# Kernel optimization log

Hardware: AMD Instinct MI355X
Metric: run time of the kernel (lower is better)

Reference implementation:

```python
import jax, jax.numpy as jnp
import numpy as np

LN_EPS = 1e-5


def _ln(x, g, b):
    m = jnp.mean(x, axis=-1, keepdims=True)
    v = jnp.mean((x - m) ** 2, axis=-1, keepdims=True)
    return (x - m) / jnp.sqrt(v + LN_EPS) * g + b


def setup_inputs() -> dict:
    key = jax.random.key(0)
    ks = jax.random.split(key, 8)
    B, N, S, D, T = 16, 64, 2048, 1024, 768

    def xavier(k, shape):
        fan_in, fan_out = shape
        lim = (6.0 / (fan_in + fan_out)) ** 0.5
        return jax.random.uniform(k, shape, minval=-lim, maxval=lim, dtype=jnp.float32)

    return {
        "prev_states": jax.random.normal(ks[0], (B, N, D), dtype=jnp.float32),
        "input_tokens": jax.random.normal(ks[1], (B, S, T), dtype=jnp.float32),
        # input_projection (token_dim -> state_dim)
        "W_proj": xavier(ks[2], (T, D)),
        "b_proj": jnp.zeros((D,), jnp.float32),
        # three LayerNorms
        "g_state": jnp.ones((D,), jnp.float32), "beta_state": jnp.zeros((D,), jnp.float32),
        "g_input": jnp.ones((D,), jnp.float32), "beta_input": jnp.zeros((D,), jnp.float32),
        "g_out": jnp.ones((D,), jnp.float32), "beta_out": jnp.zeros((D,), jnp.float32),
        # GRU gates (2D -> D); update-gate bias initialized to -1 as in the module
        "W_u": xavier(ks[3], (2 * D, D)), "b_u": jnp.full((D,), -1.0, jnp.float32),
        "W_r": xavier(ks[4], (2 * D, D)), "b_r": jnp.zeros((D,), jnp.float32),
        "W_n": xavier(ks[5], (2 * D, D)), "b_n": jnp.zeros((D,), jnp.float32),
    }


def reference(prev_states, input_tokens, W_proj, b_proj,
              g_state, beta_state, g_input, beta_input, g_out, beta_out,
              W_u, b_u, W_r, b_r, W_n, b_n):
    D = prev_states.shape[-1]
    # project tokens to state dim: (B,S,D)
    tok = input_tokens @ W_proj + b_proj
    # attention routing (routing_weights=None path)
    scores = jnp.einsum('bnd,bsd->bns', prev_states, tok) / jnp.sqrt(jnp.float32(D))
    attn = jax.nn.softmax(scores, axis=-1)
    routed = jnp.einsum('bns,bsd->bnd', attn, tok)  # (B,N,D)
    # GRU-style gated update, vectorized over the num_states axis
    ps_n = _ln(prev_states, g_state, beta_state)
    in_n = _ln(routed, g_input, beta_input)
    concat = jnp.concatenate([ps_n, in_n], axis=-1)  # (B,N,2D)
    u = jax.nn.sigmoid(concat @ W_u + b_u)
    r = jax.nn.sigmoid(concat @ W_r + b_r)
    reset_in = jnp.concatenate([r * ps_n, in_n], axis=-1)
    cand = jnp.tanh(reset_in @ W_n + b_n)  # dropout is identity in eval
    new_state = (1.0 - u) * prev_states + u * cand
    return _ln(new_state, g_out, beta_out)
```

## Files before the change

kernel.cpp:

```cpp
#include <hip/hip_runtime.h>
#include <stdint.h>

typedef __attribute__((ext_vector_type(4))) float floatx4;
typedef __attribute__((ext_vector_type(8))) short shortx8;

#define LN_EPS 1e-5f

__device__ __forceinline__ unsigned short f2b(float f) {
  unsigned u = __builtin_bit_cast(unsigned, f);
  u = (u + 0x7FFFu + ((u >> 16) & 1u)) >> 16;
  return (unsigned short)u;
}
__device__ __forceinline__ float b2f(unsigned short h) {
  return __builtin_bit_cast(float, (unsigned)h << 16);
}

__device__ __forceinline__ void g2l16(const unsigned short* g, unsigned short* l) {
  __builtin_amdgcn_global_load_lds(
      (const __attribute__((address_space(1))) unsigned int*)g,
      (__attribute__((address_space(3))) unsigned int*)l, 16, 0, 0);
}

__device__ __forceinline__ float wave_sum(float v) {
#pragma unroll
  for (int o = 32; o; o >>= 1) v += __shfl_down(v, o, 64);
  return v;
}
__device__ __forceinline__ float block_sum(float v, float* s) {
  v = wave_sum(v);
  __syncthreads();
  if ((threadIdx.x & 63) == 0) s[threadIdx.x >> 6] = v;
  __syncthreads();
  return s[0] + s[1] + s[2] + s[3];
}

__global__ __launch_bounds__(256) void k_prep_pw(
    const float* __restrict__ prev, const float* __restrict__ wp,
    const float* __restrict__ Wu, const float* __restrict__ Wr,
    const float* __restrict__ Wn,
    unsigned short* __restrict__ Wtur, unsigned short* __restrict__ Wtn,
    unsigned short* __restrict__ Wtp, unsigned short* __restrict__ pwb,
    float* __restrict__ rs) {
  __shared__ unsigned short As[2][64 * 64];
  __shared__ unsigned short Bs[2][64 * 64];
  const int bid = blockIdx.x;
  const int tid = threadIdx.x;
  if (bid < 192) {
    const int wave = tid >> 6, lane = tid & 63;
    const int swz = (bid & 7) * 24 + (bid >> 3);
    const int m0 = (swz % 16) * 64;
    const int n0 = (swz / 16) * 64;
    const int wm = wave & 1, wn = wave >> 1;
    const int l16 = lane & 15, quad = lane >> 4;
    const int srow8 = lane >> 3;
    const int c8 = ((lane & 7) ^ srow8) * 8;

    const float* gAf[2];
    const float* gBf[2];
    int lOff[2];
#pragma unroll
    for (int j = 0; j < 2; j++) {
      const int rb = wave * 16 + j * 8;
      gAf[j] = prev + (long)(m0 + rb + srow8) * 1024 + c8;
      gBf[j] = wp + (long)(n0 + rb + srow8) * 1024 + c8;
      lOff[j] = rb * 64;
    }
    int offA[2][2], offB[2][2];
#pragma unroll
    for (int ks = 0; ks < 2; ks++)
#pragma unroll
      for (int i = 0; i < 2; i++) {
        int r = wm * 32 + i * 16 + l16;
        offA[ks][i] = r * 64 + (((ks * 4 + quad) ^ (r & 7)) * 8);
        r = wn * 32 + i * 16 + l16;
        offB[ks][i] = r * 64 + (((ks * 4 + quad) ^ (r & 7)) * 8);
// ... 41 lines not shown
        for (int j = 0; j < 2; j++) bf[j] = *(const shortx8*)&Bs[cur][offB[ks][j]];
#pragma unroll
        for (int i = 0; i < 2; i++)
#pragma unroll
          for (int j = 0; j < 2; j++)
            acc[i][j] = __builtin_amdgcn_mfma_f32_16x16x32_bf16(af[i], bf[j], acc[i][j], 0, 0, 0);
      }
      if (t + 1 < nt) {
#pragma unroll
        for (int j = 0; j < 2; j++) {
          unsigned short ta[8], tb[8];
#pragma unroll
          for (int i = 0; i < 4; i++) {
            ta[i] = f2b(a0[j][i]); ta[4 + i] = f2b(a1[j][i]);
            tb[i] = f2b(b0[j][i]); tb[4 + i] = f2b(b1[j][i]);
          }
          *(uint4*)&As[cur ^ 1][lOff[j] + lane * 8] = *(uint4*)ta;
          *(uint4*)&Bs[cur ^ 1][lOff[j] + lane * 8] = *(uint4*)tb;
        }
      }
      __syncthreads();
    }

#pragma unroll
    for (int i = 0; i < 2; i++)
#pragma unroll
      for (int j = 0; j < 2; j++) {
        const int rbase = m0 + wm * 32 + i * 16 + quad * 4;
        const int c = n0 + wn * 32 + j * 16 + l16;
#pragma unroll
        for (int r = 0; r < 4; r++)
          pwb[(long)(rbase + r) * 768 + c] = f2b(acc[i][j][r]);
      }
    return;
  }
  float(*tile)[33] = (float(*)[33]) & As[0][0];
  if (bid == 192) {
    floatx4 z = {0.f, 0.f, 0.f, 0.f};
    *(floatx4*)(rs + tid * 4) = z;
  }
  int t = bid - 192;
  const float* in;
  unsigned short* out;
  int K, kx, ny;
  if (t < 6144) {
    const int which = t >> 11;
    const int t2 = t & 2047;
    kx = t2 & 63;
    ny = t2 >> 6;
    K = 2048;
    in = which == 0 ? Wu : (which == 1 ? Wr : Wn);
    out = which == 0 ? Wtur : (which == 1 ? Wtur + 1024 * 2048 : Wtn);
  } else {
    const int t2 = t - 6144;
    kx = t2 % 24;
    ny = t2 / 24;
    K = 768;
    in = wp;
    out = Wtp;
  }
  const int N = 1024;
  const int k0 = kx * 32, n0 = ny * 32;
  const int tx = tid & 31, ty = tid >> 5;
#pragma unroll
  for (int i = 0; i < 32; i += 8)
    tile[ty + i][tx] = in[(long)(k0 + ty + i) * N + n0 + tx];
  __syncthreads();
#pragma unroll
  for (int i = 0; i < 32; i += 8)
    out[(long)(n0 + ty + i) * K + k0 + tx] = f2b(tile[tx][ty + i]);
}

__global__ __launch_bounds__(256) void k_gemm64(
    const unsigned short* __restrict__ A, int lda,
    const unsigned short* __restrict__ Bt, int ldb,
    int K, long sCk,
    float* __restrict__ out, int ldc) {
  __shared__ unsigned short As[2][64 * 64];
  __shared__ unsigned short Bs[2][64 * 64];
  const int tid = threadIdx.x;
  const int wave = tid >> 6, lane = tid & 63;
  const int kc = blockIdx.z;
  const long koff = (long)kc * K;
  const int flat = blockIdx.x + blockIdx.y * gridDim.x;
  const int q = (gridDim.x * gridDim.y) >> 3;
  const int swz = (flat & 7) * q + (flat >> 3);
  const int m0 = (swz % gridDim.x) * 64;
  const int n0 = (swz / gridDim.x) * 64;
  const int wm = wave & 1, wn = wave >> 1;
  const int l16 = lane & 15, quad = lane >> 4;
  const int srow8 = lane >> 3;
  const int c8 = ((lane & 7) ^ srow8) * 8;

  const unsigned short* gA[2];
  const unsigned short* gB[2];
  int lOff[2];
#pragma unroll
  for (int j = 0; j < 2; j++) {
    const int rb = wave * 16 + j * 8;
    gA[j] = A + (long)(m0 + rb + srow8) * lda + c8 + koff;
    gB[j] = Bt + (long)(n0 + rb + srow8) * ldb + c8 + koff;
    lOff[j] = rb * 64;
  }
  int offA[2][2], offB[2][2];
#pragma unroll
  for (int ks = 0; ks < 2; ks++)
#pragma unroll
    for (int i = 0; i < 2; i++) {
      int r = wm * 32 + i * 16 + l16;
      offA[ks][i] = r * 64 + (((ks * 4 + quad) ^ (r & 7)) * 8);
      r = wn * 32 + i * 16 + l16;
      offB[ks][i] = r * 64 + (((ks * 4 + quad) ^ (r & 7)) * 8);
    }

  floatx4 acc[2][2] = {};

#pragma unroll
  for (int j = 0; j < 2; j++) {
    g2l16(gA[j], &As[0][lOff[j]]);
    g2l16(gB[j], &Bs[0][lOff[j]]);
  }
  __syncthreads();

  const int nt = K >> 6;
  for (int t = 0; t < nt; t++) {
    const int cur = t & 1;
    if (t + 1 < nt) {
      const int kn = (t + 1) << 6;
#pragma unroll
      for (int j = 0; j < 2; j++) {
        g2l16(gA[j] + kn, &As[cur ^ 1][lOff[j]]);
        g2l16(gB[j] + kn, &Bs[cur ^ 1][lOff[j]]);
      }
    }
#pragma unroll
    for (int ks = 0; ks < 2; ks++) {
      shortx8 af[2], bf[2];
#pragma unroll
      for (int i = 0; i < 2; i++) af[i] = *(const shortx8*)&As[cur][offA[ks][i]];
#pragma unroll
      for (int j = 0; j < 2; j++) bf[j] = *(const shortx8*)&Bs[cur][offB[ks][j]];
#pragma unroll
      for (int i = 0; i < 2; i++)
#pragma unroll
        for (int j = 0; j < 2; j++)
          acc[i][j] = __builtin_amdgcn_mfma_f32_16x16x32_bf16(af[i], bf[j], acc[i][j], 0, 0, 0);
    }
    __syncthreads();
  }

#pragma unroll
  for (int i = 0; i < 2; i++)
#pragma unroll
    for (int j = 0; j < 2; j++) {
      const int rbase = m0 + wm * 32 + i * 16 + quad * 4;
      const int c = n0 + wn * 32 + j * 16 + l16;
#pragma unroll
      for (int r = 0; r < 4; r++)
        out[(long)kc * sCk + (long)(rbase + r) * ldc + c] = acc[i][j][r];
    }
}

__global__ __launch_bounds__(256) void k_proj2_ln(
    const float* __restrict__ P0, int lda,
    const unsigned short* __restrict__ Bt, int ldb,
    int K,
    const float* __restrict__ bp, const float* __restrict__ rowsum,
    float* __restrict__ out, int ldc,
    const float* __restrict__ prev,
    const float* __restrict__ g_st, const float* __restrict__ be_st,
    unsigned short* __restrict__ conc) {
  __shared__ unsigned short As[2][64 * 64];
  __shared__ unsigned short Bs[2][64 * 64];
  const int tid = threadIdx.x;
  if (blockIdx.x >= 256) {
    float* scr = (float*)&As[0][0];
    const long r = blockIdx.x - 256;
    floatx4 v = *(const floatx4*)(prev + r * 1024 + tid * 4);
    float s1 = v[0] + v[1] + v[2] + v[3];
    float s2 = v[0] * v[0] + v[1] * v[1] + v[2] * v[2] + v[3] * v[3];
    s1 = block_sum(s1, scr);
    s2 = block_sum(s2, scr);
    const float mean = s1 * (1.0f / 1024.0f);
    const float var = s2 * (1.0f / 1024.0f) - mean * mean;
    const float rstd = rsqrtf(var + LN_EPS);
    unsigned short t4[4];
#pragma unroll
    for (int i = 0; i < 4; i++) {
      const int d = tid * 4 + i;
      t4[i] = f2b((v[i] - mean) * rstd * g_st[d] + be_st[d]);
    }
    *(uint2*)(conc + r * 2048 + tid * 4) = *(uint2*)t4;
    return;
  }
  const int wave = tid >> 6, lane = tid & 63;
  const int flat = blockIdx.x;
  const int swz = (flat & 7) * 32 + (flat >> 3);
  const int m0 = (swz % 16) * 64;
  const int n0 = (swz / 16) * 64;
  const int wm = wave & 1, wn = wave >> 1;
  const int l16 = lane & 15, quad = lane >> 4;
  const int srow8 = lane >> 3;
  const int c8 = ((lane & 7) ^ srow8) * 8;

  const float* gAf[2];
  const unsigned short* gB[2];
  int lOff[2];
#pragma unroll
  for (int j = 0; j < 2; j++) {
    const int rb = wave * 16 + j * 8;
    gAf[j] = P0 + (long)(m0 + rb + srow8) * lda + c8;
    gB[j] = Bt + (long)(n0 + rb + srow8) * ldb + c8;
    lOff[j] = rb * 64;
  }
  int offA[2][2], offB[2][2];
#pragma unroll
  for (int ks = 0; ks < 2; ks++)
#pragma unroll
    for (int i = 0; i < 2; i++) {
      int r = wm * 32 + i * 16 + l16;
      offA[ks][i] = r * 64 + (((ks * 4 + quad) ^ (r & 7)) * 8);
      r = wn * 32 + i * 16 + l16;
      offB[ks][i] = r * 64 + (((ks * 4 + quad) ^ (r & 7)) * 8);
    }

  floatx4 acc[2][2] = {};

#pragma unroll
  for (int j = 0; j < 2; j++) {
    g2l16(gB[j], &Bs[0][lOff[j]]);
    floatx4 a0 = *(const floatx4*)(gAf[j]);
    floatx4 a1 = *(const floatx4*)(gAf[j] + 4);
    floatx4 b0 = *(const floatx4*)(gAf[j] + 786432);
    floatx4 b1 = *(const floatx4*)(gAf[j] + 786432 + 4);
    unsigned short t8[8];
#pragma unroll
    for (int i = 0; i < 4; i++) { t8[i] = f2b(a0[i] + b0[i]); t8[4 + i] = f2b(a1[i] + b1[i]); }
    *(uint4*)&As[0][lOff[j] + lane * 8] = *(uint4*)t8;
  }
  __syncthreads();

  const int nt = K >> 6;
  for (int t = 0; t < nt; t++) {
    const int cur = t & 1;
    floatx4 a0[2], a1[2], p0[2], p1[2];
    if (t + 1 < nt) {
      const int kn = (t + 1) << 6;
#pragma unroll
      for (int j = 0; j < 2; j++) {
        g2l16(gB[j] + kn, &Bs[cur ^ 1][lOff[j]]);
        a0[j] = *(const floatx4*)(gAf[j] + kn);
        a1[j] = *(const floatx4*)(gAf[j] + kn + 4);
        p0[j] = *(const floatx4*)(gAf[j] + kn + 786432);
        p1[j] = *(const floatx4*)(gAf[j] + kn + 786432 + 4);
      }
    }
#pragma unroll
    for (int ks = 0; ks < 2; ks++) {
      shortx8 af[2], bf[2];
#pragma unroll
      for (int i = 0; i < 2; i++) af[i] = *(const shortx8*)&As[cur][offA[ks][i]];
#pragma unroll
      for (int j = 0; j < 2; j++) bf[j] = *(const shortx8*)&Bs[cur][offB[ks][j]];
#pragma unroll
      for (int i = 0; i < 2; i++)
#pragma unroll
        for (int j = 0; j < 2; j++)
          acc[i][j] = __builtin_amdgcn_mfma_f32_16x16x32_bf16(af[i], bf[j], acc[i][j], 0, 0, 0);
    }
    if (t + 1 < nt) {
#pragma unroll
      for (int j = 0; j < 2; j++) {
        unsigned short t8[8];
#pragma unroll
        for (int i = 0; i < 4; i++) {
          t8[i] = f2b(a0[j][i] + p0[j][i]);
          t8[4 + i] = f2b(a1[j][i] + p1[j][i]);
        }
        *(uint4*)&As[cur ^ 1][lOff[j] + lane * 8] = *(uint4*)t8;
      }
    }
    __syncthreads();
  }

#pragma unroll
  for (int i = 0; i < 2; i++)
#pragma unroll
    for (int j = 0; j < 2; j++) {
      const int rbase = m0 + wm * 32 + i * 16 + quad * 4;
      const int c = n0 + wn * 32 + j * 16 + l16;
#pragma unroll
      for (int r = 0; r < 4; r++) {
        const int row = rbase + r;
        out[(long)row * ldc + c] = acc[i][j][r] + rowsum[row] * bp[c];
      }
    }
}

__global__ __launch_bounds__(256) void k_scores(
    const unsigned short* __restrict__ A, long sAb, int lda,
    const float* __restrict__ toksf,
    int K, float scale,
    unsigned short* __restrict__ out2, int ldc, long sCb,
    float* __restrict__ rs) {
  __shared__ unsigned short As[2][64 * 64];
  __shared__ unsigned short Bs[2][64 * 64];
  const int tid = threadIdx.x;
  const int wave = tid >> 6, lane = tid & 63;
  const int b = blockIdx.z;
  const int m0 = 0, n0 = blockIdx.y * 64;
  const int wm = wave & 1, wn = wave >> 1;
  const int l16 = lane & 15, quad = lane >> 4;
  const int srow8 = lane >> 3;
  const int c8 = ((lane & 7) ^ srow8) * 8;
  const unsigned short* Ab = A + (long)b * sAb;

  const unsigned short* gA[2];
  const float* gBf[2];
  int lOff[2];
#pragma unroll
  for (int j = 0; j < 2; j++) {
    const int rb = wave * 16 + j * 8;
    gA[j] = Ab + (long)(m0 + rb + srow8) * lda + c8;
    gBf[j] = toksf + (long)b * 1572864 + (long)(n0 + rb + srow8) * 768 + c8;
    lOff[j] = rb * 64;
  }
  int offA[2][2], offB[2][2];
#pragma unroll
  for (int ks = 0; ks < 2; ks++)
#pragma unroll
    for (int i = 0; i < 2; i++) {
      int r = wm * 32 + i * 16 + l16;
      offA[ks][i] = r * 64 + (((ks * 4 + quad) ^ (r & 7)) * 8);
      r = wn * 32 + i * 16 + l16;
      offB[ks][i] = r * 64 + (((ks * 4 + quad) ^ (r & 7)) * 8);
    }

  floatx4 acc[2][2] = {};

#pragma unroll
  for (int j = 0; j < 2; j++) {
    g2l16(gA[j], &As[0][lOff[j]]);
    floatx4 v0 = *(const floatx4*)(gBf[j]);
    floatx4 v1 = *(const floatx4*)(gBf[j] + 4);
    unsigned short t8[8];
#pragma unroll
    for (int i = 0; i < 4; i++) { t8[i] = f2b(v0[i]); t8[4 + i] = f2b(v1[i]); }
    *(uint4*)&Bs[0][lOff[j] + lane * 8] = *(uint4*)t8;
  }
  __syncthreads();

  const int nt = K >> 6;
  for (int t = 0; t < nt; t++) {
    const int cur = t & 1;
    floatx4 w0[2], w1[2];
    if (t + 1 < nt) {
      const int kn = (t + 1) << 6;
#pragma unroll
      for (int j = 0; j < 2; j++) {
        g2l16(gA[j] + kn, &As[cur ^ 1][lOff[j]]);
        w0[j] = *(const floatx4*)(gBf[j] + kn);
        w1[j] = *(const floatx4*)(gBf[j] + kn + 4);
      }
    }
#pragma unroll
    for (int ks = 0; ks < 2; ks++) {
      shortx8 af[2], bf[2];
#pragma unroll
      for (int i = 0; i < 2; i++) af[i] = *(const shortx8*)&As[cur][offA[ks][i]];
#pragma unroll
      for (int j = 0; j < 2; j++) bf[j] = *(const shortx8*)&Bs[cur][offB[ks][j]];
#pragma unroll
      for (int i = 0; i < 2; i++)
#pragma unroll
        for (int j = 0; j < 2; j++)
          acc[i][j] = __builtin_amdgcn_mfma_f32_16x16x32_bf16(af[i], bf[j], acc[i][j], 0, 0, 0);
    }
    if (t + 1 < nt) {
#pragma unroll
      for (int j = 0; j < 2; j++) {
        unsigned short t8[8];
#pragma unroll
        for (int i = 0; i < 4; i++) { t8[i] = f2b(w0[j][i]); t8[4 + i] = f2b(w1[j][i]); }
        *(uint4*)&Bs[cur ^ 1][lOff[j] + lane * 8] = *(uint4*)t8;
      }
    }
    __syncthreads();
  }

#pragma unroll
  for (int i = 0; i < 2; i++) {
    float psum[4] = {0.f, 0.f, 0.f, 0.f};
#pragma unroll
    for (int j = 0; j < 2; j++) {
      const int rbase = m0 + wm * 32 + i * 16 + quad * 4;
      const int c = n0 + wn * 32 + j * 16 + l16;
#pragma unroll
      for (int r = 0; r < 4; r++) {
        const float e = expf(acc[i][j][r] * scale);
        out2[(long)b * sCb + (long)(rbase + r) * ldc + c] = f2b(e);
        psum[r] += e;
      }
    }
#pragma unroll
    for (int r = 0; r < 4; r++) {
      float s = psum[r];
      s += __shfl_xor(s, 1, 64);
      s += __shfl_xor(s, 2, 64);
      s += __shfl_xor(s, 4, 64);
      s += __shfl_xor(s, 8, 64);
      if (l16 == 0)
        atomicAdd(rs + (long)b * 64 + m0 + wm * 32 + i * 16 + quad * 4 + r, s);
    }
  }
}

__global__ __launch_bounds__(256) void k_routed_mfma(
    const unsigned short* __restrict__ attnb,
    const float* __restrict__ tokf,
    float* __restrict__ parts) {
  __shared__ unsigned short As[64 * 40];
  __shared__ unsigned short Bs[32 * 66];
  const int kc = blockIdx.x, nt = blockIdx.y, b = blockIdx.z;
  const int tid = threadIdx.x;
  const int wave = tid >> 6, lane = tid & 63;
  const int wm = wave & 1, wn = wave >> 1;
  const int l16 = lane & 15, quad = lane >> 4;
  const int n0 = nt * 64;
  const long abase = (long)b * 131072 + (long)kc * 1024;
  const long tbase = ((long)b * 2048 + (long)kc * 1024) * 768;
  const int srow = tid >> 2, skc = (tid & 3) * 8;
  const int bk = tid >> 3, bd = (tid & 7) * 8;

  floatx4 acc[2][2] = {};

  uint4 pa = *(const uint4*)(attnb + abase + (long)srow * 2048 + skc);
  floatx4 f0 = *(const floatx4*)(tokf + tbase + (long)bk * 768 + n0 + bd);
  floatx4 f1 = *(const floatx4*)(tokf + tbase + (long)bk * 768 + n0 + bd + 4);

  for (int k0 = 0; k0 < 1024; k0 += 32) {
    *(uint4*)&As[srow * 40 + skc] = pa;
    {
      unsigned short t8[8];
#pragma unroll
      for (int i = 0; i < 4; i++) { t8[i] = f2b(f0[i]); t8[4 + i] = f2b(f1[i]); }
// ... 8 lines not shown
    }
    asm volatile("s_waitcnt lgkmcnt(0)" ::: "memory");
    __builtin_amdgcn_s_barrier();
    __builtin_amdgcn_sched_barrier(0);

    shortx8 a0 = *(const shortx8*)&As[(wm * 32 + 0  + l16) * 40 + quad * 8];
    shortx8 a1 = *(const shortx8*)&As[(wm * 32 + 16 + l16) * 40 + quad * 8];
    shortx8 b0, b1;
#pragma unroll
    for (int j = 0; j < 8; j++) {
      b0[j] = *(const short*)&Bs[(quad * 8 + j) * 66 + wn * 32 + l16];
      b1[j] = *(const short*)&Bs[(quad * 8 + j) * 66 + wn * 32 + 16 + l16];
    }
    acc[0][0] = __builtin_amdgcn_mfma_f32_16x16x32_bf16(a0, b0, acc[0][0], 0, 0, 0);
    acc[0][1] = __builtin_amdgcn_mfma_f32_16x16x32_bf16(a0, b1, acc[0][1], 0, 0, 0);
    acc[1][0] = __builtin_amdgcn_mfma_f32_16x16x32_bf16(a1, b0, acc[1][0], 0, 0, 0);
    acc[1][1] = __builtin_amdgcn_mfma_f32_16x16x32_bf16(a1, b1, acc[1][1], 0, 0, 0);
    __builtin_amdgcn_s_barrier();
  }

#pragma unroll
  for (int im = 0; im < 2; im++)
#pragma unroll
    for (int in_ = 0; in_ < 2; in_++) {
      const int rbase = wm * 32 + im * 16 + quad * 4;
      const int c = n0 + wn * 32 + in_ * 16 + l16;
#pragma unroll
      for (int r = 0; r < 4; r++)
        parts[(long)kc * 786432 + ((long)b * 64 + rbase + r) * 768 + c] =
            acc[im][in_][r];
    }
}

__global__ __launch_bounds__(256) void k_ln_routed(
    const float* __restrict__ routed,
    const float* __restrict__ g_in, const float* __restrict__ be_in,
    unsigned short* __restrict__ conc, unsigned short* __restrict__ candA) {
  __shared__ float scr[4];
  const long r = blockIdx.x;
  const int t = threadIdx.x;
  floatx4 v = *(const floatx4*)(routed + r * 1024 + t * 4);
  float s1 = v[0] + v[1] + v[2] + v[3];
  float s2 = v[0] * v[0] + v[1] * v[1] + v[2] * v[2] + v[3] * v[3];
  s1 = block_sum(s1, scr);
  s2 = block_sum(s2, scr);
  const float mean = s1 * (1.0f / 1024.0f);
  const float var = s2 * (1.0f / 1024.0f) - mean * mean;
  const float rstd = rsqrtf(var + LN_EPS);
  unsigned short t4[4];
#pragma unroll
  for (int i = 0; i < 4; i++) {
    const int d = t * 4 + i;
    t4[i] = f2b((v[i] - mean) * rstd * g_in[d] + be_in[d]);
  }
  *(uint2*)(conc + r * 2048 + 1024 + t * 4) = *(uint2*)t4;
  *(uint2*)(candA + r * 2048 + 1024 + t * 4) = *(uint2*)t4;
}

__global__ __launch_bounds__(256) void k_gate_epi(
    const float* __restrict__ gparts,
    const float* __restrict__ bu, const float* __restrict__ br,
    const unsigned short* __restrict__ conc,
    float* __restrict__ ubuf, unsigned short* __restrict__ candA) {
  const int row = blockIdx.x >> 1;
  const int half = blockIdx.x & 1;
  const int t = threadIdx.x;
  const long base = (long)row * 2048 + half * 1024 + t * 4;
  floatx4 p0 = *(const floatx4*)(gparts + base);
  floatx4 p1 = *(const floatx4*)(gparts + 2097152 + base);
  const float* bias = half ? br : bu;
  floatx4 bv = *(const floatx4*)(bias + t * 4);
  if (!half) {
    floatx4 o;
#pragma unroll
    for (int i = 0; i < 4; i++)
      o[i] = 1.0f / (1.0f + expf(-(p0[i] + p1[i] + bv[i])));
    *(floatx4*)(ubuf + (long)row * 1024 + t * 4) = o;
  } else {
    unsigned short t4[4];
#pragma unroll
    for (int i = 0; i < 4; i++) {
      float rr = 1.0f / (1.0f + expf(-(p0[i] + p1[i] + bv[i])));
      t4[i] = f2b(rr * b2f(conc[(long)row * 2048 + t * 4 + i]));
    }
    *(uint2*)(candA + (long)row * 2048 + t * 4) = *(uint2*)t4;
  }
}

__global__ __launch_bounds__(256) void k_ln_out(
    const float* __restrict__ cparts,
    const float* __restrict__ ubuf, const float* __restrict__ prev,
    const float* __restrict__ bn,
    const float* __restrict__ g, const float* __restrict__ be,
    float* __restrict__ out) {
  __shared__ float scr[4];
  const long r = blockIdx.x;
  const int t = threadIdx.x;
  floatx4 p0 = *(const floatx4*)(cparts + r * 1024 + t * 4);
  floatx4 p1 = *(const floatx4*)(cparts + 1048576 + r * 1024 + t * 4);
  floatx4 uu = *(const floatx4*)(ubuf + r * 1024 + t * 4);
  floatx4 pv = *(const floatx4*)(prev + r * 1024 + t * 4);
  floatx4 bv = *(const floatx4*)(bn + t * 4);
  floatx4 v;
#pragma unroll
  for (int i = 0; i < 4; i++) {
    const float cand = tanhf(p0[i] + p1[i] + bv[i]);
    v[i] = (1.0f - uu[i]) * pv[i] + uu[i] * cand;
  }
  float s1 = v[0] + v[1] + v[2] + v[3];
  float s2 = v[0] * v[0] + v[1] * v[1] + v[2] * v[2] + v[3] * v[3];
  s1 = block_sum(s1, scr);
  s2 = block_sum(s2, scr);
  const float mean = s1 * (1.0f / 1024.0f);
  const float var = s2 * (1.0f / 1024.0f) - mean * mean;
  const float rstd = rsqrtf(var + LN_EPS);
  floatx4 o;
#pragma unroll
  for (int i = 0; i < 4; i++) {
    const int d = t * 4 + i;
    o[i] = (v[i] - mean) * rstd * g[d] + be[d];
  }
// ... 4 lines not shown
                              void* d_out, int out_size, void* d_ws, size_t ws_size,
                              hipStream_t stream) {
  (void)in_sizes; (void)n_in; (void)out_size; (void)ws_size;
  const float* prev  = (const float*)d_in[0];
  const float* toks  = (const float*)d_in[1];
  const float* Wp    = (const float*)d_in[2];
  const float* bp    = (const float*)d_in[3];
  const float* g_st  = (const float*)d_in[4];
  const float* be_st = (const float*)d_in[5];
  const float* g_in  = (const float*)d_in[6];
  const float* be_in = (const float*)d_in[7];
  const float* g_o   = (const float*)d_in[8];
  const float* be_o  = (const float*)d_in[9];
  const float* Wu    = (const float*)d_in[10];
  const float* bu    = (const float*)d_in[11];
  const float* Wr    = (const float*)d_in[12];
  const float* br    = (const float*)d_in[13];
  const float* Wn    = (const float*)d_in[14];
  const float* bn    = (const float*)d_in[15];
  float* out = (float*)d_out;

  char* ws = (char*)d_ws;
  unsigned short* Wtp   = (unsigned short*)ws; ws += 1572864;
  unsigned short* pwb   = (unsigned short*)ws; ws += 1572864;
  unsigned short* attnb = (unsigned short*)ws; ws += 4194304;
  float*          rowsum= (float*)ws;          ws += 4096;
  float*          parts = (float*)ws;          ws += 6291456;
  float*          routed= (float*)ws;          ws += 4194304;
  unsigned short* conc  = (unsigned short*)ws; ws += 4194304;
  unsigned short* candA = (unsigned short*)ws; ws += 4194304;
  float*          ubuf  = (float*)ws;          ws += 4194304;
  unsigned short* Wtur  = (unsigned short*)ws; ws += 8388608;
  unsigned short* Wtn   = (unsigned short*)ws; ws += 4194304;
  float*          gparts= (float*)ws;          ws += 16777216;
  float*          cparts= (float*)ws;          ws += 8388608;

  const dim3 blk(256);

  k_prep_pw<<<dim3(7104), blk, 0, stream>>>(prev, Wp, Wu, Wr, Wn,
                                            Wtur, Wtn, Wtp, pwb, rowsum);
  k_scores<<<dim3(1, 32, 16), blk, 0, stream>>>(
      pwb, 49152L, 768, toks, 768, 0.03125f,
      attnb, 2048, 131072L, rowsum);
  k_routed_mfma<<<dim3(2, 12, 16), blk, 0, stream>>>(attnb, toks, parts);
  k_proj2_ln<<<dim3(1280), blk, 0, stream>>>(
      parts, 768, Wtp, 768, 768, bp, rowsum, routed, 1024,
      prev, g_st, be_st, conc);
  k_ln_routed<<<dim3(1024), blk, 0, stream>>>(routed, g_in, be_in, conc, candA);
  k_gemm64<<<dim3(16, 32, 2), blk, 0, stream>>>(
      conc, 2048, Wtur, 2048, 1024, 2097152L, gparts, 2048);
  k_gate_epi<<<dim3(2048), blk, 0, stream>>>(gparts, bu, br, conc, ubuf, candA);
  k_gemm64<<<dim3(16, 16, 2), blk, 0, stream>>>(
      candA, 2048, Wtn, 2048, 1024, 1048576L, cparts, 1024);
  k_ln_out<<<dim3(1024), blk, 0, stream>>>(cparts, ubuf, prev, bn, g_o, be_o, out);
}
```

Measured before the change: 294.8 us.

## Reschedule split-K GRU GEMM halves into earlier kernels to overlap independent work

The state LayerNorm moves into the prep kernel. The first K-half of the gate GEMM (the normalized-state half, which does not depend on routing) now runs inside the scores kernel as extra blocks. The second K-half of the gate GEMM and of the candidate GEMM are fused into one launch before the gate epilogue, and the remaining candidate half runs afterward. This spreads GEMM work across launches that were underfilling the GPU and reduces serialized small launches. The cost is heterogeneous blocks in shared kernels and more complex dependency ordering.

```diff
diff --git a/kernel.cpp b/kernel.cpp
--- a/kernel.cpp
+++ b/kernel.cpp
@@ -34,13 +34,101 @@
   return s[0] + s[1] + s[2] + s[3];
 }
 
+__device__ __forceinline__ void gemm64_body(
+    unsigned short (*As)[64 * 64], unsigned short (*Bs)[64 * 64],
+    const unsigned short* __restrict__ A, int lda,
+    const unsigned short* __restrict__ Bt, int ldb,
+    int K, int mtiles, int total, int g,
+    float* __restrict__ out, int ldc) {
+  const int tid = threadIdx.x;
+  const int wave = tid >> 6, lane = tid & 63;
+  const int q = total >> 3;
+  const int swz = (g & 7) * q + (g >> 3);
+  const int m0 = (swz % mtiles) * 64;
+  const int n0 = (swz / mtiles) * 64;
+  const int wm = wave & 1, wn = wave >> 1;
+  const int l16 = lane & 15, quad = lane >> 4;
+  const int srow8 = lane >> 3;
+  const int c8 = ((lane & 7) ^ srow8) * 8;
+
+  const unsigned short* gA[2];
+  const unsigned short* gB[2];
+  int lOff[2];
+#pragma unroll
+  for (int j = 0; j < 2; j++) {
+    const int rb = wave * 16 + j * 8;
+    gA[j] = A + (long)(m0 + rb + srow8) * lda + c8;
+    gB[j] = Bt + (long)(n0 + rb + srow8) * ldb + c8;
+    lOff[j] = rb * 64;
+  }
+  int offA[2][2], offB[2][2];
+#pragma unroll
+  for (int ks = 0; ks < 2; ks++)
+#pragma unroll
+    for (int i = 0; i < 2; i++) {
+      int r = wm * 32 + i * 16 + l16;
+      offA[ks][i] = r * 64 + (((ks * 4 + quad) ^ (r & 7)) * 8);
+      r = wn * 32 + i * 16 + l16;
+      offB[ks][i] = r * 64 + (((ks * 4 + quad) ^ (r & 7)) * 8);
+    }
+
+  floatx4 acc[2][2] = {};
+
+#pragma unroll
+  for (int j = 0; j < 2; j++) {
+    g2l16(gA[j], &As[0][lOff[j]]);
+    g2l16(gB[j], &Bs[0][lOff[j]]);
+  }
+  __syncthreads();
+
+  const int nt = K >> 6;
+  for (int t = 0; t < nt; t++) {
+    const int cur = t & 1;
+    if (t + 1 < nt) {
+      const int kn = (t + 1) << 6;
+#pragma unroll
+      for (int j = 0; j < 2; j++) {
+        g2l16(gA[j] + kn, &As[cur ^ 1][lOff[j]]);
+        g2l16(gB[j] + kn, &Bs[cur ^ 1][lOff[j]]);
+      }
+    }
+#pragma unroll
+    for (int ks = 0; ks < 2; ks++) {
+      shortx8 af[2], bf[2];
+#pragma unroll
+      for (int i = 0; i < 2; i++) af[i] = *(const shortx8*)&As[cur][offA[ks][i]];
+#pragma unroll
+      for (int j = 0; j < 2; j++) bf[j] = *(const shortx8*)&Bs[cur][offB[ks][j]];
+#pragma unroll
+      for (int i = 0; i < 2; i++)
+#pragma unroll
+        for (int j = 0; j < 2; j++)
+          acc[i][j] = __builtin_amdgcn_mfma_f32_16x16x32_bf16(af[i], bf[j], acc[i][j], 0, 0, 0);
+    }
+    __syncthreads();
+  }
+
+#pragma unroll
+  for (int i = 0; i < 2; i++)
+#pragma unroll
+    for (int j = 0; j < 2; j++) {
+      const int rbase = m0 + wm * 32 + i * 16 + quad * 4;
+      const int c = n0 + wn * 32 + j * 16 + l16;
+#pragma unroll
+      for (int r = 0; r < 4; r++)
+        out[(long)(rbase + r) * ldc + c] = acc[i][j][r];
+    }
+}
+
 __global__ __launch_bounds__(256) void k_prep_pw(
     const float* __restrict__ prev, const float* __restrict__ wp,
     const float* __restrict__ Wu, const float* __restrict__ Wr,
     const float* __restrict__ Wn,
     unsigned short* __restrict__ Wtur, unsigned short* __restrict__ Wtn,
     unsigned short* __restrict__ Wtp, unsigned short* __restrict__ pwb,
-    float* __restrict__ rs) {
+    float* __restrict__ rs,
+    const float* __restrict__ g_st, const float* __restrict__ be_st,
+    unsigned short* __restrict__ conc) {
   __shared__ unsigned short As[2][64 * 64];
   __shared__ unsigned short Bs[2][64 * 64];
   const int bid = blockIdx.x;
@@ -148,6 +236,26 @@
         for (int r = 0; r < 4; r++)
           pwb[(long)(rbase + r) * 768 + c] = f2b(acc[i][j][r]);
       }
+    return;
+  }
+  if (bid >= 7104) {
+    float* scr = (float*)&As[0][0];
+    const long r = bid - 7104;
+    floatx4 v = *(const floatx4*)(prev + r * 1024 + tid * 4);
+    float s1 = v[0] + v[1] + v[2] + v[3];
+    float s2 = v[0] * v[0] + v[1] * v[1] + v[2] * v[2] + v[3] * v[3];
+    s1 = block_sum(s1, scr);
+    s2 = block_sum(s2, scr);
+    const float mean = s1 * (1.0f / 1024.0f);
+    const float var = s2 * (1.0f / 1024.0f) - mean * mean;
+    const float rstd = rsqrtf(var + LN_EPS);
+    unsigned short t4[4];
+#pragma unroll
+    for (int i = 0; i < 4; i++) {
+      const int d = tid * 4 + i;
+      t4[i] = f2b((v[i] - mean) * rstd * g_st[d] + be_st[d]);
+    }
+    *(uint2*)(conc + r * 2048 + tid * 4) = *(uint2*)t4;
     return;
   }
   float(*tile)[33] = (float(*)[33]) & As[0][0];
@@ -187,35 +295,38 @@
     out[(long)(n0 + ty + i) * K + k0 + tx] = f2b(tile[tx][ty + i]);
 }
 
-__global__ __launch_bounds__(256) void k_gemm64(
-    const unsigned short* __restrict__ A, int lda,
-    const unsigned short* __restrict__ Bt, int ldb,
-    int K, long sCk,
-    float* __restrict__ out, int ldc) {
+__global__ __launch_bounds__(256) void k_scores_g0(
+    const unsigned short* __restrict__ pwb,
+    const float* __restrict__ toksf,
+    unsigned short* __restrict__ attnb, float* __restrict__ rs,
+    const unsigned short* __restrict__ conc,
+    const unsigned short* __restrict__ Wtur,
+    float* __restrict__ gparts) {
   __shared__ unsigned short As[2][64 * 64];
   __shared__ unsigned short Bs[2][64 * 64];
   const int tid = threadIdx.x;
+  if (blockIdx.x >= 512) {
+    gemm64_body(As, Bs, conc, 2048, Wtur, 2048, 1024, 16, 512,
+                blockIdx.x - 512, gparts, 2048);
+    return;
+  }
   const int wave = tid >> 6, lane = tid & 63;
-  const int kc = blockIdx.z;
-  const long koff = (long)kc * K;
-  const int flat = blockIdx.x + blockIdx.y * gridDim.x;
-  const int q = (gridDim.x * gridDim.y) >> 3;
-  const int swz = (flat & 7) * q + (flat >> 3);
-  const int m0 = (swz % gridDim.x) * 64;
-  const int n0 = (swz / gridDim.x) * 64;
+  const int b = blockIdx.x >> 5;
+  const int n0 = (blockIdx.x & 31) * 64;
   const int wm = wave & 1, wn = wave >> 1;
   const int l16 = lane & 15, quad = lane >> 4;
   const int srow8 = lane >> 3;
   const int c8 = ((lane & 7) ^ srow8) * 8;
+  const unsigned short* Ab = pwb + (long)b * 49152;
 
   const unsigned short* gA[2];
-  const unsigned short* gB[2];
+  const float* gBf[2];
   int lOff[2];
 #pragma unroll
   for (int j = 0; j < 2; j++) {
     const int rb = wave * 16 + j * 8;
-    gA[j] = A + (long)(m0 + rb + srow8) * lda + c8 + koff;
-    gB[j] = Bt + (long)(n0 + rb + srow8) * ldb + c8 + koff;
+    gA[j] = Ab + (long)(rb + srow8) * 768 + c8;
+    gBf[j] = toksf + (long)b * 1572864 + (long)(n0 + rb + srow8) * 768 + c8;
     lOff[j] = rb * 64;
   }
   int offA[2][2], offB[2][2];
@@ -234,229 +345,6 @@
 #pragma unroll
   for (int j = 0; j < 2; j++) {
     g2l16(gA[j], &As[0][lOff[j]]);
-    g2l16(gB[j], &Bs[0][lOff[j]]);
-  }
-  __syncthreads();
-
-  const int nt = K >> 6;
-  for (int t = 0; t < nt; t++) {
-    const int cur = t & 1;
-    if (t + 1 < nt) {
-      const int kn = (t + 1) << 6;
-#pragma unroll
-      for (int j = 0; j < 2; j++) {
-        g2l16(gA[j] + kn, &As[cur ^ 1][lOff[j]]);
-        g2l16(gB[j] + kn, &Bs[cur ^ 1][lOff[j]]);
-      }
-    }
-#pragma unroll
-    for (int ks = 0; ks < 2; ks++) {
-      shortx8 af[2], bf[2];
-#pragma unroll
-      for (int i = 0; i < 2; i++) af[i] = *(const shortx8*)&As[cur][offA[ks][i]];
-#pragma unroll
-      for (int j = 0; j < 2; j++) bf[j] = *(const shortx8*)&Bs[cur][offB[ks][j]];
-#pragma unroll
-      for (int i = 0; i < 2; i++)
-#pragma unroll
-        for (int j = 0; j < 2; j++)
-          acc[i][j] = __builtin_amdgcn_mfma_f32_16x16x32_bf16(af[i], bf[j], acc[i][j], 0, 0, 0);
-    }
-    __syncthreads();
-  }
-
-#pragma unroll
-  for (int i = 0; i < 2; i++)
-#pragma unroll
-    for (int j = 0; j < 2; j++) {
-      const int rbase = m0 + wm * 32 + i * 16 + quad * 4;
-      const int c = n0 + wn * 32 + j * 16 + l16;
-#pragma unroll
-      for (int r = 0; r < 4; r++)
-        out[(long)kc * sCk + (long)(rbase + r) * ldc + c] = acc[i][j][r];
-    }
-}
-
-__global__ __launch_bounds__(256) void k_proj2_ln(
-    const float* __restrict__ P0, int lda,
-    const unsigned short* __restrict__ Bt, int ldb,
-    int K,
-    const float* __restrict__ bp, const float* __restrict__ rowsum,
-    float* __restrict__ out, int ldc,
-    const float* __restrict__ prev,
-    const float* __restrict__ g_st, const float* __restrict__ be_st,
-    unsigned short* __restrict__ conc) {
-  __shared__ unsigned short As[2][64 * 64];
-  __shared__ unsigned short Bs[2][64 * 64];
-  const int tid = threadIdx.x;
-  if (blockIdx.x >= 256) {
-    float* scr = (float*)&As[0][0];
-    const long r = blockIdx.x - 256;
-    floatx4 v = *(const floatx4*)(prev + r * 1024 + tid * 4);
-    float s1 = v[0] + v[1] + v[2] + v[3];
-    float s2 = v[0] * v[0] + v[1] * v[1] + v[2] * v[2] + v[3] * v[3];
-    s1 = block_sum(s1, scr);
-    s2 = block_sum(s2, scr);
-    const float mean = s1 * (1.0f / 1024.0f);
-    const float var = s2 * (1.0f / 1024.0f) - mean * mean;
-    const float rstd = rsqrtf(var + LN_EPS);
-    unsigned short t4[4];
-#pragma unroll
-    for (int i = 0; i < 4; i++) {
-      const int d = tid * 4 + i;
-      t4[i] = f2b((v[i] - mean) * rstd * g_st[d] + be_st[d]);
-    }
-    *(uint2*)(conc + r * 2048 + tid * 4) = *(uint2*)t4;
-    return;
-  }
-  const int wave = tid >> 6, lane = tid & 63;
-  const int flat = blockIdx.x;
-  const int swz = (flat & 7) * 32 + (flat >> 3);
-  const int m0 = (swz % 16) * 64;
-  const int n0 = (swz / 16) * 64;
-  const int wm = wave & 1, wn = wave >> 1;
-  const int l16 = lane & 15, quad = lane >> 4;
-  const int srow8 = lane >> 3;
-  const int c8 = ((lane & 7) ^ srow8) * 8;
-
-  const float* gAf[2];
-  const unsigned short* gB[2];
-  int lOff[2];
-#pragma unroll
-  for (int j = 0; j < 2; j++) {
-    const int rb = wave * 16 + j * 8;
-    gAf[j] = P0 + (long)(m0 + rb + srow8) * lda + c8;
-    gB[j] = Bt + (long)(n0 + rb + srow8) * ldb + c8;
-    lOff[j] = rb * 64;
-  }
-  int offA[2][2], offB[2][2];
-#pragma unroll
-  for (int ks = 0; ks < 2; ks++)
-#pragma unroll
-    for (int i = 0; i < 2; i++) {
-      int r = wm * 32 + i * 16 + l16;
-      offA[ks][i] = r * 64 + (((ks * 4 + quad) ^ (r & 7)) * 8);
-      r = wn * 32 + i * 16 + l16;
-      offB[ks][i] = r * 64 + (((ks * 4 + quad) ^ (r & 7)) * 8);
-    }
-
-  floatx4 acc[2][2] = {};
-
-#pragma unroll
-  for (int j = 0; j < 2; j++) {
-    g2l16(gB[j], &Bs[0][lOff[j]]);
-    floatx4 a0 = *(const floatx4*)(gAf[j]);
-    floatx4 a1 = *(const floatx4*)(gAf[j] + 4);
-    floatx4 b0 = *(const floatx4*)(gAf[j] + 786432);
-    floatx4 b1 = *(const floatx4*)(gAf[j] + 786432 + 4);
-    unsigned short t8[8];
-#pragma unroll
-    for (int i = 0; i < 4; i++) { t8[i] = f2b(a0[i] + b0[i]); t8[4 + i] = f2b(a1[i] + b1[i]); }
-    *(uint4*)&As[0][lOff[j] + lane * 8] = *(uint4*)t8;
-  }
-  __syncthreads();
-
-  const int nt = K >> 6;
-  for (int t = 0; t < nt; t++) {
-    const int cur = t & 1;
-    floatx4 a0[2], a1[2], p0[2], p1[2];
-    if (t + 1 < nt) {
-      const int kn = (t + 1) << 6;
-#pragma unroll
-      for (int j = 0; j < 2; j++) {
-        g2l16(gB[j] + kn, &Bs[cur ^ 1][lOff[j]]);
-        a0[j] = *(const floatx4*)(gAf[j] + kn);
-        a1[j] = *(const floatx4*)(gAf[j] + kn + 4);
-        p0[j] = *(const floatx4*)(gAf[j] + kn + 786432);
-        p1[j] = *(const floatx4*)(gAf[j] + kn + 786432 + 4);
-      }
-    }
-#pragma unroll
-    for (int ks = 0; ks < 2; ks++) {
-      shortx8 af[2], bf[2];
-#pragma unroll
-      for (int i = 0; i < 2; i++) af[i] = *(const shortx8*)&As[cur][offA[ks][i]];
-#pragma unroll
-      for (int j = 0; j < 2; j++) bf[j] = *(const shortx8*)&Bs[cur][offB[ks][j]];
-#pragma unroll
-      for (int i = 0; i < 2; i++)
-#pragma unroll
-        for (int j = 0; j < 2; j++)
-          acc[i][j] = __builtin_amdgcn_mfma_f32_16x16x32_bf16(af[i], bf[j], acc[i][j], 0, 0, 0);
-    }
-    if (t + 1 < nt) {
-#pragma unroll
-      for (int j = 0; j < 2; j++) {
-        unsigned short t8[8];
-#pragma unroll
-        for (int i = 0; i < 4; i++) {
-          t8[i] = f2b(a0[j][i] + p0[j][i]);
-          t8[4 + i] = f2b(a1[j][i] + p1[j][i]);
-        }
-        *(uint4*)&As[cur ^ 1][lOff[j] + lane * 8] = *(uint4*)t8;
-      }
-    }
-    __syncthreads();
-  }
-
-#pragma unroll
-  for (int i = 0; i < 2; i++)
-#pragma unroll
-    for (int j = 0; j < 2; j++) {
-      const int rbase = m0 + wm * 32 + i * 16 + quad * 4;
-      const int c = n0 + wn * 32 + j * 16 + l16;
-#pragma unroll
-      for (int r = 0; r < 4; r++) {
-        const int row = rbase + r;
-        out[(long)row * ldc + c] = acc[i][j][r] + rowsum[row] * bp[c];
-      }
-    }
-}
-
-__global__ __launch_bounds__(256) void k_scores(
-    const unsigned short* __restrict__ A, long sAb, int lda,
-    const float* __restrict__ toksf,
-    int K, float scale,
-    unsigned short* __restrict__ out2, int ldc, long sCb,
-    float* __restrict__ rs) {
-  __shared__ unsigned short As[2][64 * 64];
-  __shared__ unsigned short Bs[2][64 * 64];
-  const int tid = threadIdx.x;
-  const int wave = tid >> 6, lane = tid & 63;
-  const int b = blockIdx.z;
-  const int m0 = 0, n0 = blockIdx.y * 64;
-  const int wm = wave & 1, wn = wave >> 1;
-  const int l16 = lane & 15, quad = lane >> 4;
-  const int srow8 = lane >> 3;
-  const int c8 = ((lane & 7) ^ srow8) * 8;
-  const unsigned short* Ab = A + (long)b * sAb;
-
-  const unsigned short* gA[2];
-  const float* gBf[2];
-  int lOff[2];
-#pragma unroll
-  for (int j = 0; j < 2; j++) {
-    const int rb = wave * 16 + j * 8;
-    gA[j] = Ab + (long)(m0 + rb + srow8) * lda + c8;
-    gBf[j] = toksf + (long)b * 1572864 + (long)(n0 + rb + srow8) * 768 + c8;
-    lOff[j] = rb * 64;
-  }
-  int offA[2][2], offB[2][2];
-#pragma unroll
-  for (int ks = 0; ks < 2; ks++)
-#pragma unroll
-    for (int i = 0; i < 2; i++) {
-      int r = wm * 32 + i * 16 + l16;
-      offA[ks][i] = r * 64 + (((ks * 4 + quad) ^ (r & 7)) * 8);
-      r = wn * 32 + i * 16 + l16;
-      offB[ks][i] = r * 64 + (((ks * 4 + quad) ^ (r & 7)) * 8);
-    }
-
-  floatx4 acc[2][2] = {};
-
-#pragma unroll
-  for (int j = 0; j < 2; j++) {
-    g2l16(gA[j], &As[0][lOff[j]]);
     floatx4 v0 = *(const floatx4*)(gBf[j]);
     floatx4 v1 = *(const floatx4*)(gBf[j] + 4);
     unsigned short t8[8];
@@ -466,7 +354,7 @@
   }
   __syncthreads();
 
-  const int nt = K >> 6;
+  const int nt = 12;
   for (int t = 0; t < nt; t++) {
     const int cur = t & 1;
     floatx4 w0[2], w1[2];
@@ -509,12 +397,12 @@
     float psum[4] = {0.f, 0.f, 0.f, 0.f};
 #pragma unroll
     for (int j = 0; j < 2; j++) {
-      const int rbase = m0 + wm * 32 + i * 16 + quad * 4;
+      const int rbase = wm * 32 + i * 16 + quad * 4;
       const int c = n0 + wn * 32 + j * 16 + l16;
 #pragma unroll
       for (int r = 0; r < 4; r++) {
-        const float e = expf(acc[i][j][r] * scale);
-        out2[(long)b * sCb + (long)(rbase + r) * ldc + c] = f2b(e);
+        const float e = expf(acc[i][j][r] * 0.03125f);
+        attnb[(long)b * 131072 + (long)(rbase + r) * 2048 + c] = f2b(e);
         psum[r] += e;
       }
     }
@@ -526,7 +414,7 @@
       s += __shfl_xor(s, 4, 64);
       s += __shfl_xor(s, 8, 64);
       if (l16 == 0)
-        atomicAdd(rs + (long)b * 64 + m0 + wm * 32 + i * 16 + quad * 4 + r, s);
+        atomicAdd(rs + (long)b * 64 + wm * 32 + i * 16 + quad * 4 + r, s);
     }
   }
 }
@@ -601,6 +489,119 @@
     }
 }
 
+__global__ __launch_bounds__(256) void k_proj2(
+    const float* __restrict__ P0, int lda,
+    const unsigned short* __restrict__ Bt, int ldb,
+    int K,
+    const float* __restrict__ bp, const float* __restrict__ rowsum,
+    float* __restrict__ out, int ldc) {
+  __shared__ unsigned short As[2][64 * 64];
+  __shared__ unsigned short Bs[2][64 * 64];
+  const int tid = threadIdx.x;
+  const int wave = tid >> 6, lane = tid & 63;
+  const int flat = blockIdx.x;
+  const int swz = (flat & 7) * 32 + (flat >> 3);
+  const int m0 = (swz % 16) * 64;
+  const int n0 = (swz / 16) * 64;
+  const int wm = wave & 1, wn = wave >> 1;
+  const int l16 = lane & 15, quad = lane >> 4;
+  const int srow8 = lane >> 3;
+  const int c8 = ((lane & 7) ^ srow8) * 8;
+
+  const float* gAf[2];
+  const unsigned short* gB[2];
+  int lOff[2];
+#pragma unroll
+  for (int j = 0; j < 2; j++) {
+    const int rb = wave * 16 + j * 8;
+    gAf[j] = P0 + (long)(m0 + rb + srow8) * lda + c8;
+    gB[j] = Bt + (long)(n0 + rb + srow8) * ldb + c8;
+    lOff[j] = rb * 64;
+  }
+  int offA[2][2], offB[2][2];
+#pragma unroll
+  for (int ks = 0; ks < 2; ks++)
+#pragma unroll
+    for (int i = 0; i < 2; i++) {
+      int r = wm * 32 + i * 16 + l16;
+      offA[ks][i] = r * 64 + (((ks * 4 + quad) ^ (r & 7)) * 8);
+      r = wn * 32 + i * 16 + l16;
+      offB[ks][i] = r * 64 + (((ks * 4 + quad) ^ (r & 7)) * 8);
+    }
+
+  floatx4 acc[2][2] = {};
+
+#pragma unroll
+  for (int j = 0; j < 2; j++) {
+    g2l16(gB[j], &Bs[0][lOff[j]]);
+    floatx4 a0 = *(const floatx4*)(gAf[j]);
+    floatx4 a1 = *(const floatx4*)(gAf[j] + 4);
+    floatx4 b0 = *(const floatx4*)(gAf[j] + 786432);
+    floatx4 b1 = *(const floatx4*)(gAf[j] + 786432 + 4);
+    unsigned short t8[8];
+#pragma unroll
+    for (int i = 0; i < 4; i++) { t8[i] = f2b(a0[i] + b0[i]); t8[4 + i] = f2b(a1[i] + b1[i]); }
+    *(uint4*)&As[0][lOff[j] + lane * 8] = *(uint4*)t8;
+  }
+  __syncthreads();
+
+  const int nt = K >> 6;
+  for (int t = 0; t < nt; t++) {
+    const int cur = t & 1;
+    floatx4 a0[2], a1[2], p0[2], p1[2];
+    if (t + 1 < nt) {
+      const int kn = (t + 1) << 6;
+#pragma unroll
+      for (int j = 0; j < 2; j++) {
+        g2l16(gB[j] + kn, &Bs[cur ^ 1][lOff[j]]);
+        a0[j] = *(const floatx4*)(gAf[j] + kn);
+        a1[j] = *(const floatx4*)(gAf[j] + kn + 4);
+        p0[j] = *(const floatx4*)(gAf[j] + kn + 786432);
+        p1[j] = *(const floatx4*)(gAf[j] + kn + 786432 + 4);
+      }
+    }
+#pragma unroll
+    for (int ks = 0; ks < 2; ks++) {
+      shortx8 af[2], bf[2];
+#pragma unroll
+      for (int i = 0; i < 2; i++) af[i] = *(const shortx8*)&As[cur][offA[ks][i]];
+#pragma unroll
+      for (int j = 0; j < 2; j++) bf[j] = *(const shortx8*)&Bs[cur][offB[ks][j]];
+#pragma unroll
+      for (int i = 0; i < 2; i++)
+#pragma unroll
+        for (int j = 0; j < 2; j++)
+          acc[i][j] = __builtin_amdgcn_mfma_f32_16x16x32_bf16(af[i], bf[j], acc[i][j], 0, 0, 0);
+    }
+    if (t + 1 < nt) {
+#pragma unroll
+      for (int j = 0; j < 2; j++) {
+        unsigned short t8[8];
+#pragma unroll
+        for (int i = 0; i < 4; i++) {
+          t8[i] = f2b(a0[j][i] + p0[j][i]);
+          t8[4 + i] = f2b(a1[j][i] + p1[j][i]);
+        }
+        *(uint4*)&As[cur ^ 1][lOff[j] + lane * 8] = *(uint4*)t8;
+      }
+    }
+    __syncthreads();
+  }
+
+#pragma unroll
+  for (int i = 0; i < 2; i++)
+#pragma unroll
+    for (int j = 0; j < 2; j++) {
+      const int rbase = m0 + wm * 32 + i * 16 + quad * 4;
+      const int c = n0 + wn * 32 + j * 16 + l16;
+#pragma unroll
+      for (int r = 0; r < 4; r++) {
+        const int row = rbase + r;
+        out[(long)row * ldc + c] = acc[i][j][r] + rowsum[row] * bp[c];
+      }
+    }
+}
+
 __global__ __launch_bounds__(256) void k_ln_routed(
     const float* __restrict__ routed,
     const float* __restrict__ g_in, const float* __restrict__ be_in,
@@ -626,6 +627,22 @@
   *(uint2*)(candA + r * 2048 + 1024 + t * 4) = *(uint2*)t4;
 }
 
+__global__ __launch_bounds__(256) void k_g1_c2(
+    const unsigned short* __restrict__ conc,
+    const unsigned short* __restrict__ Wtur, float* __restrict__ gparts,
+    const unsigned short* __restrict__ candA,
+    const unsigned short* __restrict__ Wtn, float* __restrict__ cparts) {
+  __shared__ unsigned short As[2][64 * 64];
+  __shared__ unsigned short Bs[2][64 * 64];
+  if (blockIdx.x < 512) {
+    gemm64_body(As, Bs, conc + 1024, 2048, Wtur + 1024, 2048, 1024, 16, 512,
+                blockIdx.x, gparts + 2097152, 2048);
+  } else {
+    gemm64_body(As, Bs, candA + 1024, 2048, Wtn + 1024, 2048, 1024, 16, 256,
+                blockIdx.x - 512, cparts + 1048576, 1024);
+  }
+}
+
 __global__ __launch_bounds__(256) void k_gate_epi(
     const float* __restrict__ gparts,
     const float* __restrict__ bu, const float* __restrict__ br,
@@ -654,6 +671,15 @@
     }
     *(uint2*)(candA + (long)row * 2048 + t * 4) = *(uint2*)t4;
   }
+}
+
+__global__ __launch_bounds__(256) void k_cand1(
+    const unsigned short* __restrict__ candA,
+    const unsigned short* __restrict__ Wtn, float* __restrict__ cparts) {
+  __shared__ unsigned short As[2][64 * 64];
+  __shared__ unsigned short Bs[2][64 * 64];
+  gemm64_body(As, Bs, candA, 2048, Wtn, 2048, 1024, 16, 256,
+              blockIdx.x, cparts, 1024);
 }
 
 __global__ __launch_bounds__(256) void k_ln_out(
@@ -731,20 +757,17 @@
 
   const dim3 blk(256);
 
-  k_prep_pw<<<dim3(7104), blk, 0, stream>>>(prev, Wp, Wu, Wr, Wn,
-                                            Wtur, Wtn, Wtp, pwb, rowsum);
-  k_scores<<<dim3(1, 32, 16), blk, 0, stream>>>(
-      pwb, 49152L, 768, toks, 768, 0.03125f,
-      attnb, 2048, 131072L, rowsum);
+  k_prep_pw<<<dim3(8128), blk, 0, stream>>>(prev, Wp, Wu, Wr, Wn,
+                                            Wtur, Wtn, Wtp, pwb, rowsum,
+                                            g_st, be_st, conc);
+  k_scores_g0<<<dim3(1024), blk, 0, stream>>>(pwb, toks, attnb, rowsum,
+                                              conc, Wtur, gparts);
   k_routed_mfma<<<dim3(2, 12, 16), blk, 0, stream>>>(attnb, toks, parts);
-  k_proj2_ln<<<dim3(1280), blk, 0, stream>>>(
-      parts, 768, Wtp, 768, 768, bp, rowsum, routed, 1024,
-      prev, g_st, be_st, conc);
+  k_proj2<<<dim3(256), blk, 0, stream>>>(parts, 768, Wtp, 768, 768,
+                                         bp, rowsum, routed, 1024);
   k_ln_routed<<<dim3(1024), blk, 0, stream>>>(routed, g_in, be_in, conc, candA);
-  k_gemm64<<<dim3(16, 32, 2), blk, 0, stream>>>(
-      conc, 2048, Wtur, 2048, 1024, 2097152L, gparts, 2048);
+  k_g1_c2<<<dim3(768), blk, 0, stream>>>(conc, Wtur, gparts, candA, Wtn, cparts);
   k_gate_epi<<<dim3(2048), blk, 0, stream>>>(gparts, bu, br, conc, ubuf, candA);
-  k_gemm64<<<dim3(16, 16, 2), blk, 0, stream>>>(
-      candA, 2048, Wtn, 2048, 1024, 1048576L, cparts, 1024);
+  k_cand1<<<dim3(256), blk, 0, stream>>>(candA, Wtn, cparts);
   k_ln_out<<<dim3(1024), blk, 0, stream>>>(cparts, ubuf, prev, bn, g_o, be_o, out);
 }
```

After: 302.7 us. 1.03x slower.

## Fuse gate GEMM with sigmoid epilogue and drop split-K partials

Applied to the files above, without the earlier changes.

Replaces the split-K gate GEMM (two K-chunks writing fp32 partials) plus the separate gate epilogue kernel with one GEMM kernel that runs the full K=2048 and applies bias, sigmoid and the reset-times-state product in its epilogue. This removes the 16 MB partial buffer round trip and one launch. In exchange the grid shrinks from 1024 to 512 blocks, each running a K loop twice as long, which may lower occupancy and parallelism. The epilogue stores are also scalar and strided rather than vectorised.

```diff
diff --git a/kernel.cpp b/kernel.cpp
--- a/kernel.cpp
+++ b/kernel.cpp
@@ -185,6 +185,105 @@
 #pragma unroll
   for (int i = 0; i < 32; i += 8)
     out[(long)(n0 + ty + i) * K + k0 + tx] = f2b(tile[tx][ty + i]);
+}
+
+__global__ __launch_bounds__(256) void k_gates5(
+    const unsigned short* __restrict__ conc,
+    const unsigned short* __restrict__ Wtur,
+    const float* __restrict__ bu, const float* __restrict__ br,
+    float* __restrict__ ubuf, unsigned short* __restrict__ candA) {
+  __shared__ unsigned short As[2][64 * 64];
+  __shared__ unsigned short Bs[2][64 * 64];
+  const int tid = threadIdx.x;
+  const int wave = tid >> 6, lane = tid & 63;
+  const int flat = blockIdx.x + blockIdx.y * gridDim.x;
+  const int q = (gridDim.x * gridDim.y) >> 3;
+  const int swz = (flat & 7) * q + (flat >> 3);
+  const int m0 = (swz % gridDim.x) * 64;
+  const int n0 = (swz / gridDim.x) * 64;
+  const int wm = wave & 1, wn = wave >> 1;
+  const int l16 = lane & 15, quad = lane >> 4;
+  const int srow8 = lane >> 3;
+  const int c8 = ((lane & 7) ^ srow8) * 8;
+
+  const unsigned short* gA[2];
+  const unsigned short* gB[2];
+  int lOff[2];
+#pragma unroll
+  for (int j = 0; j < 2; j++) {
+    const int rb = wave * 16 + j * 8;
+    gA[j] = conc + (long)(m0 + rb + srow8) * 2048 + c8;
+    gB[j] = Wtur + (long)(n0 + rb + srow8) * 2048 + c8;
+    lOff[j] = rb * 64;
+  }
+  int offA[2][2], offB[2][2];
+#pragma unroll
+  for (int ks = 0; ks < 2; ks++)
+#pragma unroll
+    for (int i = 0; i < 2; i++) {
+      int r = wm * 32 + i * 16 + l16;
+      offA[ks][i] = r * 64 + (((ks * 4 + quad) ^ (r & 7)) * 8);
+      r = wn * 32 + i * 16 + l16;
+      offB[ks][i] = r * 64 + (((ks * 4 + quad) ^ (r & 7)) * 8);
+    }
+
+  floatx4 acc[2][2] = {};
+
+#pragma unroll
+  for (int j = 0; j < 2; j++) {
+    g2l16(gA[j], &As[0][lOff[j]]);
+    g2l16(gB[j], &Bs[0][lOff[j]]);
+  }
+  __syncthreads();
+
+  const int nt = 32;
+  for (int t = 0; t < nt; t++) {
+    const int cur = t & 1;
+    if (t + 1 < nt) {
+      const int kn = (t + 1) << 6;
+#pragma unroll
+      for (int j = 0; j < 2; j++) {
+        g2l16(gA[j] + kn, &As[cur ^ 1][lOff[j]]);
+        g2l16(gB[j] + kn, &Bs[cur ^ 1][lOff[j]]);
+      }
+    }
+#pragma unroll
+    for (int ks = 0; ks < 2; ks++) {
+      shortx8 af[2], bf[2];
+#pragma unroll
+      for (int i = 0; i < 2; i++) af[i] = *(const shortx8*)&As[cur][offA[ks][i]];
+#pragma unroll
+      for (int j = 0; j < 2; j++) bf[j] = *(const shortx8*)&Bs[cur][offB[ks][j]];
+#pragma unroll
+      for (int i = 0; i < 2; i++)
+#pragma unroll
+        for (int j = 0; j < 2; j++)
+          acc[i][j] = __builtin_amdgcn_mfma_f32_16x16x32_bf16(af[i], bf[j], acc[i][j], 0, 0, 0);
+    }
+    __syncthreads();
+  }
+
+#pragma unroll
+  for (int i = 0; i < 2; i++)
+#pragma unroll
+    for (int j = 0; j < 2; j++) {
+      const int rbase = m0 + wm * 32 + i * 16 + quad * 4;
+      const int c = n0 + wn * 32 + j * 16 + l16;
+#pragma unroll
+      for (int r = 0; r < 4; r++) {
+        const int row = rbase + r;
+        if (c < 1024) {
+          const float v = acc[i][j][r] + bu[c];
+          ubuf[(long)row * 1024 + c] = 1.0f / (1.0f + expf(-v));
+        } else {
+          const int cc = c - 1024;
+          const float v = acc[i][j][r] + br[cc];
+          const float rr = 1.0f / (1.0f + expf(-v));
+          candA[(long)row * 2048 + cc] =
+              f2b(rr * b2f(conc[(long)row * 2048 + cc]));
+        }
+      }
+    }
 }
 
 __global__ __launch_bounds__(256) void k_gemm64(
@@ -626,36 +725,6 @@
   *(uint2*)(candA + r * 2048 + 1024 + t * 4) = *(uint2*)t4;
 }
 
-__global__ __launch_bounds__(256) void k_gate_epi(
-    const float* __restrict__ gparts,
-    const float* __restrict__ bu, const float* __restrict__ br,
-    const unsigned short* __restrict__ conc,
-    float* __restrict__ ubuf, unsigned short* __restrict__ candA) {
-  const int row = blockIdx.x >> 1;
-  const int half = blockIdx.x & 1;
-  const int t = threadIdx.x;
-  const long base = (long)row * 2048 + half * 1024 + t * 4;
-  floatx4 p0 = *(const floatx4*)(gparts + base);
-  floatx4 p1 = *(const floatx4*)(gparts + 2097152 + base);
-  const float* bias = half ? br : bu;
-  floatx4 bv = *(const floatx4*)(bias + t * 4);
-  if (!half) {
-    floatx4 o;
-#pragma unroll
-    for (int i = 0; i < 4; i++)
-      o[i] = 1.0f / (1.0f + expf(-(p0[i] + p1[i] + bv[i])));
-    *(floatx4*)(ubuf + (long)row * 1024 + t * 4) = o;
-  } else {
-    unsigned short t4[4];
-#pragma unroll
-    for (int i = 0; i < 4; i++) {
-      float rr = 1.0f / (1.0f + expf(-(p0[i] + p1[i] + bv[i])));
-      t4[i] = f2b(rr * b2f(conc[(long)row * 2048 + t * 4 + i]));
-    }
-    *(uint2*)(candA + (long)row * 2048 + t * 4) = *(uint2*)t4;
-  }
-}
-
 __global__ __launch_bounds__(256) void k_ln_out(
     const float* __restrict__ cparts,
     const float* __restrict__ ubuf, const float* __restrict__ prev,
@@ -726,7 +795,6 @@
   float*          ubuf  = (float*)ws;          ws += 4194304;
   unsigned short* Wtur  = (unsigned short*)ws; ws += 8388608;
   unsigned short* Wtn   = (unsigned short*)ws; ws += 4194304;
-  float*          gparts= (float*)ws;          ws += 16777216;
   float*          cparts= (float*)ws;          ws += 8388608;
 
   const dim3 blk(256);
@@ -741,9 +809,7 @@
       parts, 768, Wtp, 768, 768, bp, rowsum, routed, 1024,
       prev, g_st, be_st, conc);
   k_ln_routed<<<dim3(1024), blk, 0, stream>>>(routed, g_in, be_in, conc, candA);
-  k_gemm64<<<dim3(16, 32, 2), blk, 0, stream>>>(
-      conc, 2048, Wtur, 2048, 1024, 2097152L, gparts, 2048);
-  k_gate_epi<<<dim3(2048), blk, 0, stream>>>(gparts, bu, br, conc, ubuf, candA);
+  k_gates5<<<dim3(16, 32), blk, 0, stream>>>(conc, Wtur, bu, br, ubuf, candA);
   k_gemm64<<<dim3(16, 16, 2), blk, 0, stream>>>(
       candA, 2048, Wtn, 2048, 1024, 1048576L, cparts, 1024);
   k_ln_out<<<dim3(1024), blk, 0, stream>>>(cparts, ubuf, prev, bn, g_o, be_o, out);
```

New measurement: 300.7 us. Within noise of the previous version (+2.0%).
